# Optimization experiments

Hardware: AMD Instinct MI355X
Metric: run time of the kernel (lower is better)

The kernel has to match this reference:

```python
import jax, jax.numpy as jnp
import numpy as np

B, N = 2, 200
IMG = 2048
NC = 4                    # node concepts ('Is*')
NODE_CH = NC * 256        # 1024
EC = 3                    # edge concepts minus 'HigherPri'
AC = 4                    # actions
BBOX_MAX = 1024.0
E = N * (N - 1)

# static fully-connected directed edge list (src=i, dst=j, i!=j), row-major order
_ii, _jj = np.meshgrid(np.arange(N), np.arange(N), indexing='ij')
_m = _ii != _jj
SRC = jnp.asarray(_ii[_m])
DST = jnp.asarray(_jj[_m])


def _lin(k, fin, fout):
    kw, kb = jax.random.split(k)
    s = 1.0 / np.sqrt(fin)
    return (jax.random.uniform(kw, (fin, fout), jnp.float32, -s, s),
            jax.random.uniform(kb, (fout,), jnp.float32, -s, s))


def setup_inputs():
    ks = jax.random.split(jax.random.key(0), 16)
    p = {}
    p['roi_features'] = jax.random.normal(ks[0], (B, N, IMG), jnp.float32)
    p['batch_bboxes'] = jax.random.uniform(ks[1], (B, N, 4), jnp.float32) * BBOX_MAX
    p['batch_directions'] = jax.random.normal(ks[2], (B, N, 4), jnp.float32)
    p['batch_priorities'] = jax.random.normal(ks[3], (B, N), jnp.float32)
    p['w1'], p['b1'] = _lin(ks[4], IMG, 512)
    p['w2'], p['b2'] = _lin(ks[5], 512, 256)
    p['w3'], p['b3'] = _lin(ks[6], 256, NODE_CH)
    p['wi'], p['bi'] = _lin(ks[7], NODE_CH, NC)
    p['we1'], p['be1'] = _lin(ks[8], 16, 256)
    p['we2'], p['be2'] = _lin(ks[9], 256, 64)
    p['we3'], p['be3'] = _lin(ks[10], 64, EC)
    p['wp1'], p['bp1'] = _lin(ks[11], EC + 1, 128)
    p['wp2'], p['bp2'] = _lin(ks[12], 128, NODE_CH * AC)
    p['root_w'], _ = _lin(ks[13], NODE_CH, AC)
    _, p['root_b'] = _lin(ks[14], NODE_CH, AC)
    return p


def reference(roi_features, batch_bboxes, batch_directions, batch_priorities,
              w1, b1, w2, b2, w3, b3, wi, bi,
              we1, be1, we2, be2, we3, be3,
              wp1, bp1, wp2, bp2, root_w, root_b):
    # node concept embedding MLP: [B,N,IMG] -> [B,N,NODE_CH]
    h = jax.nn.relu(roi_features @ w1 + b1)
    h = jax.nn.relu(h @ w2 + b2)
    node_concepts = h @ w3 + b3
    node_concepts_explicit = jax.nn.sigmoid(node_concepts @ wi + bi)

    # pairwise attributes for all directed edges (same ordering as torch masks)
    node_attr = jnp.concatenate([batch_bboxes / BBOX_MAX, batch_directions], -1)  # [B,N,8]
    pair = jnp.concatenate([node_attr[:, SRC], node_attr[:, DST]], -1)            # [B,E,16]
    eh = jax.nn.relu(pair @ we1 + be1)
    eh = jax.nn.relu(eh @ we2 + be2)
    edge_attributes = jax.nn.sigmoid(eh @ we3 + be3)                              # [B,E,EC]
    higher_pri = (batch_priorities[:, SRC] > batch_priorities[:, DST]).astype(jnp.float32)
    edge_attributes = jnp.concatenate([edge_attributes, higher_pri[..., None]], -1)  # [B,E,EC+1]

    # NNConv on graph 0: per-edge weight matrix, gather-matmul-scatter
    x = node_concepts[0]                 # [N, NODE_CH]
    e = edge_attributes[0]               # [E, EC+1]
    w = jax.nn.relu(e @ wp1 + bp1) @ wp2 + bp2
    w = w.reshape(E, NODE_CH, AC)        # [E, NODE_CH, AC]
    msg = jnp.einsum('ei,eio->eo', x[SRC], w)          # [E, AC]
    agg = jax.ops.segment_sum(msg, DST, num_segments=N)  # [N, AC]
    next_actions = agg + x @ root_w + root_b
    return (next_actions, node_concepts_explicit[0], edge_attributes[0])
```

## Files before the change

kernel.cpp:

```cpp
#include <hip/hip_runtime.h>
#include <math.h>

#define NN 200
#define ETOT 39800

typedef float float4v __attribute__((ext_vector_type(4)));
typedef short short8 __attribute__((ext_vector_type(8)));
typedef unsigned int uint4v __attribute__((ext_vector_type(4)));

__device__ __forceinline__ float sigf(float x) { return 1.0f / (1.0f + expf(-x)); }

__device__ __forceinline__ unsigned short f2b(float f) {
  unsigned u = __float_as_uint(f);
  u += 0x7fffu + ((u >> 16) & 1u);
  return (unsigned short)(u >> 16);
}
__device__ __forceinline__ unsigned pk2(float a, float b) {
  unsigned r;
  asm("v_cvt_pk_bf16_f32 %0, %1, %2" : "=v"(r) : "v"(a), "v"(b));
  return r;
}
__device__ __forceinline__ float4v mfma16(short8 a, short8 b, float4v c) {
  return __builtin_amdgcn_mfma_f32_16x16x32_bf16(a, b, c, 0, 0, 0);
}

union SharedU {
  float trans[64][65];
  float red[4][16][34];
};

template <int KSTEPS>
__device__ __forceinline__ float tile_core(const unsigned short* __restrict__ A,
                                           const unsigned short* __restrict__ B,
                                           int m0, int n0, int K, float (&red)[4][16][34]) {
  const int tid = threadIdx.x, lane = tid & 63, wv = tid >> 6;
  const int mr = lane & 15, quad = lane >> 4;
  const unsigned short* Ap = A + (size_t)(m0 + mr) * K + wv * (KSTEPS * 32) + quad * 8;
  const unsigned short* Bp = B + (size_t)(n0 + mr) * K + wv * (KSTEPS * 32) + quad * 8;
  float4v acc0 = {0.f, 0.f, 0.f, 0.f}, acc1 = {0.f, 0.f, 0.f, 0.f};
#pragma unroll
  for (int s = 0; s < KSTEPS; s += 2) {
    acc0 = mfma16(*(const short8*)(Ap + s * 32), *(const short8*)(Bp + s * 32), acc0);
    acc1 = mfma16(*(const short8*)(Ap + (s + 1) * 32), *(const short8*)(Bp + (s + 1) * 32), acc1);
  }
  float4v acc = acc0 + acc1;
#pragma unroll
  for (int r = 0; r < 4; ++r) red[wv][quad * 4 + r][mr] = acc[r];
  __syncthreads();
  const int row = tid >> 4, col = tid & 15;
  return red[0][row][col] + red[1][row][col] + red[2][row][col] + red[3][row][col];
}

template <int KSTEPS>
__device__ __forceinline__ void tile_core2(const unsigned short* __restrict__ A,
                                           const unsigned short* __restrict__ B,
                                           int m0, int n0, int K,
                                           float& v0, float& v1, float (&red)[4][16][34]) {
  const int tid = threadIdx.x, lane = tid & 63, wv = tid >> 6;
  const int mr = lane & 15, quad = lane >> 4;
  const unsigned short* Ap = A + (size_t)(m0 + mr) * K + wv * (KSTEPS * 32) + quad * 8;
  const unsigned short* B0 = B + (size_t)(n0 + mr) * K + wv * (KSTEPS * 32) + quad * 8;
  const unsigned short* B1 = B0 + (size_t)16 * K;
  float4v a0 = {0.f, 0.f, 0.f, 0.f}, a1 = {0.f, 0.f, 0.f, 0.f};
#pragma unroll
  for (int s = 0; s < KSTEPS; ++s) {
    short8 af = *(const short8*)(Ap + s * 32);
    a0 = mfma16(af, *(const short8*)(B0 + s * 32), a0);
    a1 = mfma16(af, *(const short8*)(B1 + s * 32), a1);
  }
#pragma unroll
  for (int r = 0; r < 4; ++r) {
    red[wv][quad * 4 + r][mr] = a0[r];
    red[wv][quad * 4 + r][17 + mr] = a1[r];
  }
  __syncthreads();
  const int row = tid >> 4, col = tid & 15;
  v0 = red[0][row][col] + red[1][row][col] + red[2][row][col] + red[3][row][col];
  v1 = red[0][row][17 + col] + red[1][row][17 + col] + red[2][row][17 + col] + red[3][row][17 + col];
}

__global__ __launch_bounds__(256) void k_prep(
    const float* __restrict__ w1, const float* __restrict__ roi,
    unsigned short* __restrict__ w1T, unsigned short* __restrict__ roiB) {
  __shared__ float lds[64][65];
  const int b = blockIdx.x, tid = threadIdx.x;
  if (b < 256) {
    const int kt = b % 32, nt = b / 32;
#pragma unroll 4
    for (int i = 0; i < 16; ++i) {
      int idx = tid + i * 256, r = idx >> 6, c = idx & 63;
      lds[r][c] = w1[(size_t)(kt * 64 + r) * 512 + nt * 64 + c];
    }
    __syncthreads();
#pragma unroll 4
    for (int i = 0; i < 16; ++i) {
      int idx = tid + i * 256, r = idx >> 6, c = idx & 63;
      w1T[(size_t)(nt * 64 + r) * 2048 + kt * 64 + c] = f2b(lds[c][r]);
    }
  } else {
    int n = b - 256;
    const float4v* R4 = (const float4v*)(roi + (size_t)n * 2048);
    unsigned long long* O = (unsigned long long*)(roiB + (size_t)n * 2048);
#pragma unroll
    for (int j = 0; j < 2; ++j) {
      int idx = tid + j * 256;
      float4v v = R4[idx];
      union { unsigned u[2]; unsigned long long ll; } pk;
      pk.u[0] = pk2(v[0], v[1]);
      pk.u[1] = pk2(v[2], v[3]);
      O[idx] = pk.ll;
    }
  }
}

__global__ __launch_bounds__(256) void k_g1x(
    const unsigned short* __restrict__ roiB, const unsigned short* __restrict__ w1T,
    const float* __restrict__ b1, unsigned short* __restrict__ h1,
    const float* __restrict__ w2, unsigned short* __restrict__ w2T,
    const float* __restrict__ wp2, const float* __restrict__ wi,
    const float* __restrict__ rootw, const float* __restrict__ bp2,
    unsigned short* __restrict__ Ac,
    const float* __restrict__ w3, const float* __restrict__ b3, unsigned short* __restrict__ Bc,
    const float* __restrict__ we2, unsigned short* __restrict__ we2T,
    const float* __restrict__ bbox, const float* __restrict__ dir,
    const float* __restrict__ we1, const float* __restrict__ be1,
    float* __restrict__ P, float* __restrict__ Q,
    const float* __restrict__ wp1, float* __restrict__ wp1T) {
  __shared__ SharedU sh;
  const int t = blockIdx.x, tid = threadIdx.x;
  if (t < 416) {
    const int m0 = (t % 13) * 16, n0 = (t / 13) * 16;
    float v = tile_core<16>(roiB, w1T, m0, n0, 2048, sh.red);
    const int row = tid >> 4, col = tid & 15;
    v += b1[n0 + col];
    v = fmaxf(v, 0.f);
    h1[(size_t)(m0 + row) * 512 + n0 + col] = f2b(v);
  } else if (t < 448) {
    const int tt = t - 416, kt = tt % 8, nt = tt / 8;
#pragma unroll 4
    for (int i = 0; i < 16; ++i) {
      int idx = tid + i * 256, r = idx >> 6, c = idx & 63;
      sh.trans[r][c] = w2[(size_t)(kt * 64 + r) * 256 + nt * 64 + c];
    }
    __syncthreads();
#pragma unroll 4
    for (int i = 0; i < 16; ++i) {
      int idx = tid + i * 256, r = idx >> 6, c = idx & 63;
      w2T[(size_t)(nt * 64 + r) * 512 + kt * 64 + c] = f2b(sh.trans[c][r]);
    }
  } else if (t < 576) {
    int k = t - 448;
    int o = tid >> 6, l = tid & 63;
    const float* src = wp2 + (size_t)k * 4096;
    unsigned short* dst = Ac + (size_t)(k * 4 + o) * 1024;
    for (int i = l; i < 1024; i += 64) dst[i] = f2b(src[i * 4 + o]);
  } else if (t < 592) {
    int r = t - 576;
    unsigned short* dst = Ac + (size_t)(512 + r) * 1024;
    const float* src = (r < 4) ? (wi + r) : (r < 8) ? (rootw + (r - 4))
                     : (r < 12) ? (bp2 + (r - 8)) : nullptr;
    for (int i = tid; i < 1024; i += 256)
      dst[i] = src ? f2b(src[i * 4]) : (unsigned short)0;
  } else if (t < 664) {
    int rb = (t - 592) * 4;
#pragma unroll
    for (int j = 0; j < 16; ++j) {
      int idx = tid + j * 256;
      int row = rb + (idx >> 10), i = idx & 1023;
      float val = (row < 256) ? w3[(size_t)row * 1024 + i] : (row == 256 ? b3[i] : 0.0f);
      Bc[(size_t)row * 1024 + i] = f2b(val);
    }
  } else if (t < 680) {
    int f = (t - 664) * 256 + tid;
    int c = f >> 6, k0 = (f & 63) * 4;
#pragma unroll
    for (int q = 0; q < 4; ++q)
      we2T[c * 256 + k0 + q] = f2b(we2[(k0 + q) * 64 + c]);
  } else if (t < 880) {
    int n = t - 680, c = tid;
    float aa[8];
#pragma unroll
    for (int r = 0; r < 4; ++r) aa[r] = bbox[n * 4 + r] * (1.0f / 1024.0f);
#pragma unroll
    for (int r = 0; r < 4; ++r) aa[4 + r] = dir[n * 4 + r];
    float p = be1[c], q = 0.0f;
#pragma unroll
    for (int r = 0; r < 8; ++r) {
      p += aa[r] * we1[r * 256 + c];
      q += aa[r] * we1[(8 + r) * 256 + c];
    }
    P[n * 256 + c] = p;
    Q[n * 256 + c] = q;
  } else {
    if (tid < 128) {
      float4v v = {wp1[tid], wp1[128 + tid], wp1[256 + tid], wp1[384 + tid]};
      ((float4v*)wp1T)[tid] = v;
    }
  }
}

__global__ __launch_bounds__(256) void k_g2x(
    const unsigned short* __restrict__ h1, const unsigned short* __restrict__ w2T,
    const float* __restrict__ b2, unsigned short* __restrict__ h2,
    const unsigned short* __restrict__ Ac, const unsigned short* __restrict__ Bc,
    unsigned short* __restrict__ CT, float* __restrict__ biasT) {
  __shared__ SharedU sh;
  const int t = blockIdx.x, tid = threadIdx.x;
  if (t < 208) {
    const int m0 = (t % 13) * 16, n0 = (t / 13) * 16;
    float v = tile_core<4>(h1, w2T, m0, n0, 512, sh.red);
    const int row = tid >> 4, col = tid & 15;
    v += b2[n0 + col];
    v = fmaxf(v, 0.f);
    h2[(size_t)(m0 + row) * 256 + n0 + col] = f2b(v);
  } else {
    const int u = t - 208, mi = u % 33, nj = u / 33;
    const int m0 = mi * 16, n0 = nj * 32;
    float v0, v1;
    tile_core2<8>(Ac, Bc, m0, n0, 1024, v0, v1, sh.red);
    const int row = tid >> 4, col = tid & 15;
    const int m = m0 + row;
    const int c0 = n0 + col, c1 = n0 + 16 + col;
    if (c0 < 256) CT[(size_t)m * 256 + c0] = f2b(v0);
    else if (c0 == 256) biasT[m] = v0;
    if (c1 < 256) CT[(size_t)m * 256 + c1] = f2b(v1);
  }
}

__global__ __launch_bounds__(256) void k_tfused(const unsigned short* __restrict__ h2,
                                                const unsigned short* __restrict__ CT,
                                                const float* __restrict__ biasT,
                                                const float* __restrict__ bi,
                                                const float* __restrict__ rootb,
                                                float* __restrict__ Tm, float* __restrict__ out1,
                                                float* __restrict__ out0, float* __restrict__ U) {
  __shared__ SharedU sh;
  const int m0 = blockIdx.x * 16, n0 = blockIdx.y * 16, tid = threadIdx.x;
  float v = tile_core<2>(h2, CT, m0, n0, 256, sh.red);
  const int row = tid >> 4, col = tid & 15;
  const int n = m0 + row, c = n0 + col;
  v += biasT[c];
  if (c < 512) {
    Tm[(size_t)n * 512 + c] = v;
  } else if (n < NN) {
    int r = c - 512;
    if (r < 4) out1[n * 4 + r] = sigf(v + bi[r]);
    else if (r < 8) out0[n * 4 + (r - 4)] = v + rootb[r - 4];
    else if (r < 12) U[n * 4 + (r - 8)] = v;
  }
}

__global__ __launch_bounds__(128) void k_edge(
    const float* __restrict__ P, const float* __restrict__ Q,
    const unsigned short* __restrict__ we2T,
    const float* __restrict__ be2, const float* __restrict__ we3, const float* __restrict__ be3,
    const float* __restrict__ wp1T, const float* __restrict__ bp1,
    const float* __restrict__ pri,
    const float* __restrict__ T, const float* __restrict__ U,
    float* __restrict__ out0, float* __restrict__ out_ea) {
  __shared__ int src_s[32], dst_s[32];
  __shared__ float ea_s[32][4];
  __shared__ float4v wp1s[128];
  __shared__ float bp1s[128];
  __shared__ float4v Ts[2][128];
  __shared__ float Us[2][4];

  const int tid = threadIdx.x;
  const int e0 = blockIdx.x * 32;
  const int s_lo = e0 / 199;

  if (tid < 32) {
    int e = e0 + tid;
    int i = -1, j = 0;
    if (e < ETOT) {
      i = e / 199;
      int jj = e - i * 199;
      j = jj + (jj >= i ? 1 : 0);
    }
    src_s[tid] = i;
    dst_s[tid] = j;
  }
  wp1s[tid] = ((const float4v*)wp1T)[tid];
  bp1s[tid] = bp1[tid];
#pragma unroll
  for (int j = 0; j < 2; ++j) {
    int idx = tid + j * 128;
    int row = idx >> 7, c = idx & 127;
    Ts[row][c] = ((const float4v*)T)[(s_lo + row) * 128 + c];
  }
  if (tid < 8) {
    int s = min(s_lo + (tid >> 2), 199);
    Us[tid >> 2][tid & 3] = U[s * 4 + (tid & 3)];
  }
  __syncthreads();

  const int lane = tid & 63;
  const int wv = tid >> 6;
  const int m = lane & 15;
  const int quad = lane >> 4;
  const int eloc = wv * 16 + m;
  const int si = src_s[eloc];
  const int dj = dst_s[eloc];

  float4v acc[4];
#pragma unroll
  for (int ct = 0; ct < 4; ++ct) { acc[ct][0] = 0.f; acc[ct][1] = 0.f; acc[ct][2] = 0.f; acc[ct][3] = 0.f; }

  const short8* W8 = (const short8*)we2T;

  for (int ks = 0; ks < 8; ++ks) {
    union { short8 s; uint4v u; } af;
    af.s = (short8)0;
    if (si >= 0) {
      const float4v* p4 = (const float4v*)(P + si * 256 + ks * 32 + quad * 8);
      const float4v* q4 = (const float4v*)(Q + dj * 256 + ks * 32 + quad * 8);
      float4v v0 = p4[0] + q4[0];
      float4v v1 = p4[1] + q4[1];
      af.u[0] = pk2(fmaxf(v0[0], 0.f), fmaxf(v0[1], 0.f));
      af.u[1] = pk2(fmaxf(v0[2], 0.f), fmaxf(v0[3], 0.f));
      af.u[2] = pk2(fmaxf(v1[0], 0.f), fmaxf(v1[1], 0.f));
      af.u[3] = pk2(fmaxf(v1[2], 0.f), fmaxf(v1[3], 0.f));
    }
#pragma unroll
    for (int ct = 0; ct < 4; ++ct) {
      short8 bf = W8[(ct * 16 + m) * 32 + ks * 4 + quad];
      acc[ct] = __builtin_amdgcn_mfma_f32_16x16x32_bf16(af.s, bf, acc[ct], 0, 0, 0);
    }
  }

  float ev[4][3];
#pragma unroll
  for (int r = 0; r < 4; ++r) { ev[r][0] = 0.f; ev[r][1] = 0.f; ev[r][2] = 0.f; }
#pragma unroll
  for (int ct = 0; ct < 4; ++ct) {
    const int col = ct * 16 + m;
    const float b2v = be2[col];
    const float w0 = we3[col * 3 + 0], w1v = we3[col * 3 + 1], w2v = we3[col * 3 + 2];
#pragma unroll
    for (int r = 0; r < 4; ++r) {
      float e2 = fmaxf(acc[ct][r] + b2v, 0.f);
      ev[r][0] += e2 * w0;
      ev[r][1] += e2 * w1v;
      ev[r][2] += e2 * w2v;
    }
  }
#pragma unroll
  for (int r = 0; r < 4; ++r)
#pragma unroll
    for (int p = 0; p < 3; ++p) {
      float v = ev[r][p];
      v += __shfl_xor(v, 1, 64);
      v += __shfl_xor(v, 2, 64);
      v += __shfl_xor(v, 4, 64);
      v += __shfl_xor(v, 8, 64);
      ev[r][p] = v;
    }
  if (m == 0) {
#pragma unroll
    for (int r = 0; r < 4; ++r) {
      int el = wv * 16 + quad * 4 + r;
      int ss = src_s[el], dd = dst_s[el];
      if (ss >= 0) {
        float4v o;
        o[0] = sigf(ev[r][0] + be3[0]);
        o[1] = sigf(ev[r][1] + be3[1]);
        o[2] = sigf(ev[r][2] + be3[2]);
        o[3] = (pri[ss] > pri[dd]) ? 1.0f : 0.0f;
        *(float4v*)&ea_s[el][0] = o;
        *(float4v*)(out_ea + (size_t)(e0 + el) * 4) = o;
      }
    }
  }
  __syncthreads();

  const int ee = tid >> 2, pp = tid & 3;
  const int s2 = src_s[ee], d2 = dst_s[ee];
  float4v pm = {0.f, 0.f, 0.f, 0.f};
  if (s2 >= 0) {
    const int srow = s2 - s_lo;
    const float c0 = ea_s[ee][0], c1 = ea_s[ee][1], c2 = ea_s[ee][2], c3 = ea_s[ee][3];
#pragma unroll 8
    for (int tt = pp; tt < 128; tt += 4) {
      float4v w4 = wp1s[tt];
      float hv = bp1s[tt] + c0 * w4[0] + c1 * w4[1] + c2 * w4[2] + c3 * w4[3];
      hv = fmaxf(hv, 0.f);
      pm += hv * Ts[srow][tt];
    }
  }
#pragma unroll
  for (int o = 0; o < 4; ++o) {
    float v = pm[o];
    v += __shfl_xor(v, 1, 64);
    v += __shfl_xor(v, 2, 64);
    pm[o] = v;
  }
  if (s2 >= 0) atomicAdd(&out0[d2 * 4 + pp], Us[s2 - s_lo][pp] + pm[pp]);
}

extern "C" void kernel_launch(void* const* d_in, const int* in_sizes, int n_in,
                              void* d_out, int out_size, void* d_ws, size_t ws_size,
                              hipStream_t stream) {
  (void)in_sizes; (void)n_in; (void)out_size; (void)ws_size;
  const float* roi   = (const float*)d_in[0];
  const float* bbox  = (const float*)d_in[1];
  const float* dir   = (const float*)d_in[2];
  const float* pri   = (const float*)d_in[3];
  const float* w1    = (const float*)d_in[4];
  const float* b1    = (const float*)d_in[5];
  const float* w2    = (const float*)d_in[6];
  const float* b2    = (const float*)d_in[7];
  const float* w3    = (const float*)d_in[8];
  const float* b3    = (const float*)d_in[9];
  const float* wi    = (const float*)d_in[10];
  const float* bi    = (const float*)d_in[11];
  const float* we1   = (const float*)d_in[12];
  const float* be1   = (const float*)d_in[13];
  const float* we2   = (const float*)d_in[14];
  const float* be2   = (const float*)d_in[15];
  const float* we3   = (const float*)d_in[16];
  const float* be3   = (const float*)d_in[17];
  const float* wp1   = (const float*)d_in[18];
  const float* bp1   = (const float*)d_in[19];
  const float* wp2   = (const float*)d_in[20];
  const float* bp2   = (const float*)d_in[21];
  const float* rootw = (const float*)d_in[22];
  const float* rootb = (const float*)d_in[23];

  float* out0 = (float*)d_out;
  float* out1 = out0 + 800;
  float* out2 = out0 + 1600;

  unsigned short* us = (unsigned short*)d_ws;
  unsigned short* w1T  = us;
  unsigned short* w2T  = us + 1048576;
  unsigned short* Ac   = us + 1179648;
  unsigned short* Bc   = us + 1720320;
  unsigned short* we2T = us + 2015232;
  unsigned short* roiB = us + 2031616;
  unsigned short* h1   = us + 2457600;
  unsigned short* h2   = us + 2564096;
  unsigned short* CT   = us + 2617344;
  float* fb    = (float*)(us + 2752512);
  float* Tm    = fb;
  float* Pm    = fb + 106496;
  float* Qm    = fb + 157696;
  float* Um    = fb + 208896;
  float* wp1Tp = fb + 209696;
  float* biasT = fb + 210208;

  k_prep<<<456, 256, 0, stream>>>(w1, roi, w1T, roiB);

  k_g1x<<<881, 256, 0, stream>>>(roiB, w1T, b1, h1,
                                 w2, w2T,
                                 wp2, wi, rootw, bp2, Ac,
                                 w3, b3, Bc,
                                 we2, we2T,
                                 bbox, dir, we1, be1, Pm, Qm,
                                 wp1, wp1Tp);

  k_g2x<<<505, 256, 0, stream>>>(h1, w2T, b2, h2, Ac, Bc, CT, biasT);

  k_tfused<<<dim3(13, 33), 256, 0, stream>>>(h2, CT, biasT, bi, rootb, Tm, out1, out0, Um);

  k_edge<<<1244, 128, 0, stream>>>(Pm, Qm, we2T, be2, we3, be3, wp1Tp, bp1, pri, Tm, Um, out0, out2);
}
```

Measured before the change: 157.0 us.

## Move edge MLP into earlier kernel to overlap with node GEMM

```diff
diff --git a/kernel.cpp b/kernel.cpp
--- a/kernel.cpp
+++ b/kernel.cpp
@@ -27,6 +27,7 @@
 union SharedU {
   float trans[64][65];
   float red[4][16][34];
+  struct { int src_s[64]; int dst_s[64]; } e;
 };
 
 template <int KSTEPS>
@@ -81,7 +82,11 @@
 
 __global__ __launch_bounds__(256) void k_prep(
     const float* __restrict__ w1, const float* __restrict__ roi,
-    unsigned short* __restrict__ w1T, unsigned short* __restrict__ roiB) {
+    const float* __restrict__ bbox, const float* __restrict__ dir,
+    const float* __restrict__ we1, const float* __restrict__ be1,
+    const float* __restrict__ we2,
+    unsigned short* __restrict__ w1T, unsigned short* __restrict__ roiB,
+    float* __restrict__ P, float* __restrict__ Q, unsigned short* __restrict__ we2T) {
   __shared__ float lds[64][65];
   const int b = blockIdx.x, tid = threadIdx.x;
   if (b < 256) {
@@ -97,7 +102,7 @@
       int idx = tid + i * 256, r = idx >> 6, c = idx & 63;
       w1T[(size_t)(nt * 64 + r) * 2048 + kt * 64 + c] = f2b(lds[c][r]);
     }
-  } else {
+  } else if (b < 456) {
     int n = b - 256;
     const float4v* R4 = (const float4v*)(roi + (size_t)n * 2048);
     unsigned long long* O = (unsigned long long*)(roiB + (size_t)n * 2048);
@@ -110,21 +115,42 @@
       pk.u[1] = pk2(v[2], v[3]);
       O[idx] = pk.ll;
     }
+  } else if (b < 656) {
+    int n = b - 456, c = tid;
+    float aa[8];
+#pragma unroll
+    for (int r = 0; r < 4; ++r) aa[r] = bbox[n * 4 + r] * (1.0f / 1024.0f);
+#pragma unroll
+    for (int r = 0; r < 4; ++r) aa[4 + r] = dir[n * 4 + r];
+    float p = be1[c], q = 0.0f;
+#pragma unroll
+    for (int r = 0; r < 8; ++r) {
+      p += aa[r] * we1[r * 256 + c];
+      q += aa[r] * we1[(8 + r) * 256 + c];
+    }
+    P[n * 256 + c] = p;
+    Q[n * 256 + c] = q;
+  } else {
+    int f = (b - 656) * 256 + tid;
+    int c = f >> 6, k0 = (f & 63) * 4;
+#pragma unroll
+    for (int q = 0; q < 4; ++q)
+      we2T[c * 256 + k0 + q] = f2b(we2[(k0 + q) * 64 + c]);
   }
 }
 
 __global__ __launch_bounds__(256) void k_g1x(
     const unsigned short* __restrict__ roiB, const unsigned short* __restrict__ w1T,
     const float* __restrict__ b1, unsigned short* __restrict__ h1,
+    const float* __restrict__ P, const float* __restrict__ Q,
+    const unsigned short* __restrict__ we2T,
+    const float* __restrict__ be2, const float* __restrict__ we3, const float* __restrict__ be3,
+    const float* __restrict__ pri, float* __restrict__ out_ea,
     const float* __restrict__ w2, unsigned short* __restrict__ w2T,
     const float* __restrict__ wp2, const float* __restrict__ wi,
     const float* __restrict__ rootw, const float* __restrict__ bp2,
     unsigned short* __restrict__ Ac,
     const float* __restrict__ w3, const float* __restrict__ b3, unsigned short* __restrict__ Bc,
-    const float* __restrict__ we2, unsigned short* __restrict__ we2T,
-    const float* __restrict__ bbox, const float* __restrict__ dir,
-    const float* __restrict__ we1, const float* __restrict__ be1,
-    float* __restrict__ P, float* __restrict__ Q,
     const float* __restrict__ wp1, float* __restrict__ wp1T) {
   __shared__ SharedU sh;
   const int t = blockIdx.x, tid = threadIdx.x;
@@ -135,8 +161,99 @@
     v += b1[n0 + col];
     v = fmaxf(v, 0.f);
     h1[(size_t)(m0 + row) * 512 + n0 + col] = f2b(v);
-  } else if (t < 448) {
-    const int tt = t - 416, kt = tt % 8, nt = tt / 8;
+  } else if (t < 1038) {
+    const int e0 = (t - 416) * 64;
+    if (tid < 64) {
+      int e = e0 + tid;
+      int i = -1, j = 0;
+      if (e < ETOT) {
+        i = e / 199;
+        int jj = e - i * 199;
+        j = jj + (jj >= i ? 1 : 0);
+      }
+      sh.e.src_s[tid] = i;
+      sh.e.dst_s[tid] = j;
+    }
+    __syncthreads();
+
+    const int lane = tid & 63;
+    const int wv = tid >> 6;
+    const int m = lane & 15;
+    const int quad = lane >> 4;
+    const int eloc = wv * 16 + m;
+    const int si = sh.e.src_s[eloc];
+    const int dj = sh.e.dst_s[eloc];
+
+    float4v acc[4];
+#pragma unroll
+    for (int ct = 0; ct < 4; ++ct) { acc[ct][0] = 0.f; acc[ct][1] = 0.f; acc[ct][2] = 0.f; acc[ct][3] = 0.f; }
+
+    const short8* W8 = (const short8*)we2T;
+
+    for (int ks = 0; ks < 8; ++ks) {
+      union { short8 s; uint4v u; } af;
+      af.s = (short8)0;
+      if (si >= 0) {
+        const float4v* p4 = (const float4v*)(P + si * 256 + ks * 32 + quad * 8);
+        const float4v* q4 = (const float4v*)(Q + dj * 256 + ks * 32 + quad * 8);
+        float4v v0 = p4[0] + q4[0];
+        float4v v1 = p4[1] + q4[1];
+        af.u[0] = pk2(fmaxf(v0[0], 0.f), fmaxf(v0[1], 0.f));
+        af.u[1] = pk2(fmaxf(v0[2], 0.f), fmaxf(v0[3], 0.f));
+        af.u[2] = pk2(fmaxf(v1[0], 0.f), fmaxf(v1[1], 0.f));
+        af.u[3] = pk2(fmaxf(v1[2], 0.f), fmaxf(v1[3], 0.f));
+      }
+#pragma unroll
+      for (int ct = 0; ct < 4; ++ct) {
+        short8 bf = W8[(ct * 16 + m) * 32 + ks * 4 + quad];
+        acc[ct] = __builtin_amdgcn_mfma_f32_16x16x32_bf16(af.s, bf, acc[ct], 0, 0, 0);
+      }
+    }
+
+    float ev[4][3];
+#pragma unroll
+    for (int r = 0; r < 4; ++r) { ev[r][0] = 0.f; ev[r][1] = 0.f; ev[r][2] = 0.f; }
+#pragma unroll
+    for (int ct = 0; ct < 4; ++ct) {
+      const int col = ct * 16 + m;
+      const float b2v = be2[col];
+      const float w0 = we3[col * 3 + 0], w1v = we3[col * 3 + 1], w2v = we3[col * 3 + 2];
+#pragma unroll
+      for (int r = 0; r < 4; ++r) {
+        float e2 = fmaxf(acc[ct][r] + b2v, 0.f);
+        ev[r][0] += e2 * w0;
+        ev[r][1] += e2 * w1v;
+        ev[r][2] += e2 * w2v;
+      }
+    }
+#pragma unroll
+    for (int r = 0; r < 4; ++r)
+#pragma unroll
+      for (int p = 0; p < 3; ++p) {
+        float v = ev[r][p];
+        v += __shfl_xor(v, 1, 64);
+        v += __shfl_xor(v, 2, 64);
+        v += __shfl_xor(v, 4, 64);
+        v += __shfl_xor(v, 8, 64);
+        ev[r][p] = v;
+      }
+    if (m == 0) {
+#pragma unroll
+      for (int r = 0; r < 4; ++r) {
+        int el = wv * 16 + quad * 4 + r;
+        int ss = sh.e.src_s[el], dd = sh.e.dst_s[el];
+        if (ss >= 0) {
+          float4v o;
+          o[0] = sigf(ev[r][0] + be3[0]);
+          o[1] = sigf(ev[r][1] + be3[1]);
+          o[2] = sigf(ev[r][2] + be3[2]);
+          o[3] = (pri[ss] > pri[dd]) ? 1.0f : 0.0f;
+          *(float4v*)(out_ea + (size_t)(e0 + el) * 4) = o;
+        }
+      }
+    }
+  } else if (t < 1070) {
+    const int tt = t - 1038, kt = tt % 8, nt = tt / 8;
 #pragma unroll 4
     for (int i = 0; i < 16; ++i) {
       int idx = tid + i * 256, r = idx >> 6, c = idx & 63;
@@ -148,21 +265,21 @@
       int idx = tid + i * 256, r = idx >> 6, c = idx & 63;
       w2T[(size_t)(nt * 64 + r) * 512 + kt * 64 + c] = f2b(sh.trans[c][r]);
     }
-  } else if (t < 576) {
-    int k = t - 448;
+  } else if (t < 1198) {
+    int k = t - 1070;
     int o = tid >> 6, l = tid & 63;
     const float* src = wp2 + (size_t)k * 4096;
     unsigned short* dst = Ac + (size_t)(k * 4 + o) * 1024;
     for (int i = l; i < 1024; i += 64) dst[i] = f2b(src[i * 4 + o]);
-  } else if (t < 592) {
-    int r = t - 576;
+  } else if (t < 1214) {
+    int r = t - 1198;
     unsigned short* dst = Ac + (size_t)(512 + r) * 1024;
     const float* src = (r < 4) ? (wi + r) : (r < 8) ? (rootw + (r - 4))
                      : (r < 12) ? (bp2 + (r - 8)) : nullptr;
     for (int i = tid; i < 1024; i += 256)
       dst[i] = src ? f2b(src[i * 4]) : (unsigned short)0;
-  } else if (t < 664) {
-    int rb = (t - 592) * 4;
+  } else if (t < 1286) {
+    int rb = (t - 1214) * 4;
 #pragma unroll
     for (int j = 0; j < 16; ++j) {
       int idx = tid + j * 256;
@@ -170,27 +287,6 @@
       float val = (row < 256) ? w3[(size_t)row * 1024 + i] : (row == 256 ? b3[i] : 0.0f);
       Bc[(size_t)row * 1024 + i] = f2b(val);
     }
-  } else if (t < 680) {
-    int f = (t - 664) * 256 + tid;
-    int c = f >> 6, k0 = (f & 63) * 4;
-#pragma unroll
-    for (int q = 0; q < 4; ++q)
-      we2T[c * 256 + k0 + q] = f2b(we2[(k0 + q) * 64 + c]);
-  } else if (t < 880) {
-    int n = t - 680, c = tid;
-    float aa[8];
-#pragma unroll
-    for (int r = 0; r < 4; ++r) aa[r] = bbox[n * 4 + r] * (1.0f / 1024.0f);
-#pragma unroll
-    for (int r = 0; r < 4; ++r) aa[4 + r] = dir[n * 4 + r];
-    float p = be1[c], q = 0.0f;
-#pragma unroll
-    for (int r = 0; r < 8; ++r) {
-      p += aa[r] * we1[r * 256 + c];
-      q += aa[r] * we1[(8 + r) * 256 + c];
-    }
-    P[n * 256 + c] = p;
-    Q[n * 256 + c] = q;
   } else {
     if (tid < 128) {
       float4v v = {wp1[tid], wp1[128 + tid], wp1[256 + tid], wp1[384 + tid]};
@@ -250,126 +346,44 @@
   }
 }
 
-__global__ __launch_bounds__(128) void k_edge(
-    const float* __restrict__ P, const float* __restrict__ Q,
-    const unsigned short* __restrict__ we2T,
-    const float* __restrict__ be2, const float* __restrict__ we3, const float* __restrict__ be3,
-    const float* __restrict__ wp1T, const float* __restrict__ bp1,
-    const float* __restrict__ pri,
+__global__ __launch_bounds__(256) void k_tail(
+    const float* __restrict__ ea, const float* __restrict__ wp1T, const float* __restrict__ bp1,
     const float* __restrict__ T, const float* __restrict__ U,
-    float* __restrict__ out0, float* __restrict__ out_ea) {
-  __shared__ int src_s[32], dst_s[32];
-  __shared__ float ea_s[32][4];
+    float* __restrict__ out0) {
+  __shared__ int src_s[64], dst_s[64];
+  __shared__ float4v ea_s[64];
   __shared__ float4v wp1s[128];
   __shared__ float bp1s[128];
   __shared__ float4v Ts[2][128];
   __shared__ float Us[2][4];
 
   const int tid = threadIdx.x;
-  const int e0 = blockIdx.x * 32;
+  const int e0 = blockIdx.x * 64;
   const int s_lo = e0 / 199;
 
-  if (tid < 32) {
+  if (tid < 64) {
     int e = e0 + tid;
     int i = -1, j = 0;
     if (e < ETOT) {
       i = e / 199;
       int jj = e - i * 199;
       j = jj + (jj >= i ? 1 : 0);
+      ea_s[tid] = ((const float4v*)ea)[e];
     }
     src_s[tid] = i;
     dst_s[tid] = j;
   }
-  wp1s[tid] = ((const float4v*)wp1T)[tid];
-  bp1s[tid] = bp1[tid];
-#pragma unroll
-  for (int j = 0; j < 2; ++j) {
-    int idx = tid + j * 128;
-    int row = idx >> 7, c = idx & 127;
+  if (tid < 128) {
+    wp1s[tid] = ((const float4v*)wp1T)[tid];
+    bp1s[tid] = bp1[tid];
+  }
+  {
+    int row = tid >> 7, c = tid & 127;
     Ts[row][c] = ((const float4v*)T)[(s_lo + row) * 128 + c];
   }
   if (tid < 8) {
     int s = min(s_lo + (tid >> 2), 199);
     Us[tid >> 2][tid & 3] = U[s * 4 + (tid & 3)];
-  }
-  __syncthreads();
-
-  const int lane = tid & 63;
-  const int wv = tid >> 6;
-  const int m = lane & 15;
-  const int quad = lane >> 4;
-  const int eloc = wv * 16 + m;
-  const int si = src_s[eloc];
-  const int dj = dst_s[eloc];
-
-  float4v acc[4];
-#pragma unroll
-  for (int ct = 0; ct < 4; ++ct) { acc[ct][0] = 0.f; acc[ct][1] = 0.f; acc[ct][2] = 0.f; acc[ct][3] = 0.f; }
-
-  const short8* W8 = (const short8*)we2T;
-
-  for (int ks = 0; ks < 8; ++ks) {
-    union { short8 s; uint4v u; } af;
-    af.s = (short8)0;
-    if (si >= 0) {
-      const float4v* p4 = (const float4v*)(P + si * 256 + ks * 32 + quad * 8);
-      const float4v* q4 = (const float4v*)(Q + dj * 256 + ks * 32 + quad * 8);
-      float4v v0 = p4[0] + q4[0];
-      float4v v1 = p4[1] + q4[1];
-      af.u[0] = pk2(fmaxf(v0[0], 0.f), fmaxf(v0[1], 0.f));
-      af.u[1] = pk2(fmaxf(v0[2], 0.f), fmaxf(v0[3], 0.f));
-      af.u[2] = pk2(fmaxf(v1[0], 0.f), fmaxf(v1[1], 0.f));
-      af.u[3] = pk2(fmaxf(v1[2], 0.f), fmaxf(v1[3], 0.f));
-    }
-#pragma unroll
-    for (int ct = 0; ct < 4; ++ct) {
-      short8 bf = W8[(ct * 16 + m) * 32 + ks * 4 + quad];
-      acc[ct] = __builtin_amdgcn_mfma_f32_16x16x32_bf16(af.s, bf, acc[ct], 0, 0, 0);
-    }
-  }
-
-  float ev[4][3];
-#pragma unroll
-  for (int r = 0; r < 4; ++r) { ev[r][0] = 0.f; ev[r][1] = 0.f; ev[r][2] = 0.f; }
-#pragma unroll
-  for (int ct = 0; ct < 4; ++ct) {
-    const int col = ct * 16 + m;
-    const float b2v = be2[col];
-    const float w0 = we3[col * 3 + 0], w1v = we3[col * 3 + 1], w2v = we3[col * 3 + 2];
-#pragma unroll
-    for (int r = 0; r < 4; ++r) {
-      float e2 = fmaxf(acc[ct][r] + b2v, 0.f);
-      ev[r][0] += e2 * w0;
-      ev[r][1] += e2 * w1v;
-      ev[r][2] += e2 * w2v;
-    }
-  }
-#pragma unroll
-  for (int r = 0; r < 4; ++r)
-#pragma unroll
-    for (int p = 0; p < 3; ++p) {
-      float v = ev[r][p];
-      v += __shfl_xor(v, 1, 64);
-      v += __shfl_xor(v, 2, 64);
-      v += __shfl_xor(v, 4, 64);
-      v += __shfl_xor(v, 8, 64);
-      ev[r][p] = v;
-    }
-  if (m == 0) {
-#pragma unroll
-    for (int r = 0; r < 4; ++r) {
-      int el = wv * 16 + quad * 4 + r;
-      int ss = src_s[el], dd = dst_s[el];
-      if (ss >= 0) {
-        float4v o;
-        o[0] = sigf(ev[r][0] + be3[0]);
-        o[1] = sigf(ev[r][1] + be3[1]);
-        o[2] = sigf(ev[r][2] + be3[2]);
-        o[3] = (pri[ss] > pri[dd]) ? 1.0f : 0.0f;
-        *(float4v*)&ea_s[el][0] = o;
-        *(float4v*)(out_ea + (size_t)(e0 + el) * 4) = o;
-      }
-    }
   }
   __syncthreads();
 
@@ -378,7 +392,8 @@
   float4v pm = {0.f, 0.f, 0.f, 0.f};
   if (s2 >= 0) {
     const int srow = s2 - s_lo;
-    const float c0 = ea_s[ee][0], c1 = ea_s[ee][1], c2 = ea_s[ee][2], c3 = ea_s[ee][3];
+    const float4v c4 = ea_s[ee];
+    const float c0 = c4[0], c1 = c4[1], c2 = c4[2], c3 = c4[3];
 #pragma unroll 8
     for (int tt = pp; tt < 128; tt += 4) {
       float4v w4 = wp1s[tt];
@@ -448,19 +463,19 @@
   float* wp1Tp = fb + 209696;
   float* biasT = fb + 210208;
 
-  k_prep<<<456, 256, 0, stream>>>(w1, roi, w1T, roiB);
-
-  k_g1x<<<881, 256, 0, stream>>>(roiB, w1T, b1, h1,
-                                 w2, w2T,
-                                 wp2, wi, rootw, bp2, Ac,
-                                 w3, b3, Bc,
-                                 we2, we2T,
-                                 bbox, dir, we1, be1, Pm, Qm,
-                                 wp1, wp1Tp);
+  k_prep<<<672, 256, 0, stream>>>(w1, roi, bbox, dir, we1, be1, we2,
+                                  w1T, roiB, Pm, Qm, we2T);
+
+  k_g1x<<<1287, 256, 0, stream>>>(roiB, w1T, b1, h1,
+                                  Pm, Qm, we2T, be2, we3, be3, pri, out2,
+                                  w2, w2T,
+                                  wp2, wi, rootw, bp2, Ac,
+                                  w3, b3, Bc,
+                                  wp1, wp1Tp);
 
   k_g2x<<<505, 256, 0, stream>>>(h1, w2T, b2, h2, Ac, Bc, CT, biasT);
 
   k_tfused<<<dim3(13, 33), 256, 0, stream>>>(h2, CT, biasT, bi, rootb, Tm, out1, out0, Um);
 
-  k_edge<<<1244, 128, 0, stream>>>(Pm, Qm, we2T, be2, we3, be3, wp1Tp, bp1, pri, Tm, Um, out0, out2);
-}
+  k_tail<<<622, 256, 0, stream>>>(out2, wp1Tp, bp1, Tm, Um, out0);
+}
```

After: 155.2 us. No clear change (-1.2%).
